# Performance work log

Hardware: AMD Instinct MI355X
Metric: run time of the kernel (lower is better)

## Reference

```python
import jax, jax.numpy as jnp
import numpy as np

L, N, D, B_, T = 4, 4, 2048, 2, 2048  # num_blocks, expansion_rate, dim, batch, seq


def setup_inputs() -> dict:
    key = jax.random.key(0)
    ks = jax.random.split(key, 12)
    f = lambda k, sh, s=0.02: s * jax.random.normal(k, sh, jnp.float32)
    x = jax.random.normal(ks[0], (B_, T, D), jnp.float32)
    # structural torch inits + small noise so grads/kernels are exercised
    eyecols = jnp.stack([jnp.eye(N, dtype=jnp.float32)[:, [i % N]] for i in range(L)])  # [L,N,1]
    A_m = eyecols + f(ks[1], (L, N, 1), 0.05)
    A_r = jnp.broadcast_to(jnp.eye(N, dtype=jnp.float32), (L, N, N)) + f(ks[2], (L, N, N), 0.05)
    Bp = jnp.ones((L, 1, N), jnp.float32) + f(ks[3], (L, 1, N), 0.05)
    W_m = f(ks[4], (L, D, 1))
    W_r = f(ks[5], (L, D, N))
    W_b = f(ks[6], (L, D, N))
    s_a = 0.01 * jnp.ones((L, 1, 1), jnp.float32)
    s_b = 0.01 * jnp.ones((L, 1, 1), jnp.float32)
    dyn_gamma = jnp.ones((L, D), jnp.float32) + f(ks[7], (L, D), 0.05)   # LayerNorm(bias=False)
    norm_gamma = jnp.ones((L, D), jnp.float32) + f(ks[8], (L, D), 0.05)  # per-block norm weight
    norm_beta = f(ks[9], (L, D))                                          # per-block norm bias
    Wblk = f(ks[10], (L, D, D), 1.0) / np.sqrt(D)                         # block = Linear(D, D)
    bblk = f(ks[11], (L, D))
    return dict(x=x, A_m=A_m, A_r=A_r, Bp=Bp, W_m=W_m, W_r=W_r, W_b=W_b,
                s_a=s_a, s_b=s_b, dyn_gamma=dyn_gamma, norm_gamma=norm_gamma,
                norm_beta=norm_beta, Wblk=Wblk, bblk=bblk)


def _ln(x, gamma, beta=None, eps=1e-5):
    mu = jnp.mean(x, axis=-1, keepdims=True)
    var = jnp.mean(jnp.square(x - mu), axis=-1, keepdims=True)
    y = (x - mu) * jax.lax.rsqrt(var + eps) * gamma
    return y if beta is None else y + beta


def reference(x, A_m, A_r, Bp, W_m, W_r, W_b, s_a, s_b,
              dyn_gamma, norm_gamma, norm_beta, Wblk, bblk):
    # hyper branch (n > 0), dynamic=True, pre_norm=True
    H = jnp.repeat(x[:, :, None, :], N, axis=2)  # [B,T,N,D]
    for i in range(L):
        # ---- width connections ----
        Hn = _ln(H, dyn_gamma[i])                                              # dynamic LN, no bias
        Am = A_m[i] + s_a[i] * jnp.tanh(jnp.einsum('btnd,do->btno', Hn, W_m[i]))  # [B,T,N,1]
        Ar = A_r[i] + s_a[i] * jnp.tanh(jnp.einsum('btnd,dm->btnm', Hn, W_r[i]))  # [B,T,N,N]
        WC = jnp.concatenate([Am, Ar], axis=-1)                                # [B,T,N,1+N]
        Ht = jnp.einsum('btnd,btnm->btdm', H, WC)                              # H^T @ WC
        h = Ht[..., 0]                                                         # [B,T,D]
        H = jnp.swapaxes(Ht[..., 1:], -2, -1)                                  # [B,T,N,D]
        # ---- pre-norm + block ----
        h = _ln(h, norm_gamma[i], norm_beta[i])
        h = jnp.einsum('btd,de->bte', h, Wblk[i]) + bblk[i]
        # ---- depth connections ----
        hn = _ln(h, dyn_gamma[i])
        Bv = Bp[i][0] + s_b[i] * jnp.tanh(jnp.einsum('btd,dn->btn', hn, W_b[i]))  # [B,T,N]
        H = H + h[:, :, None, :] * Bv[..., None]
    return H.sum(axis=2)  # [B,T,D]
```

## Files before the change

kernel.cpp:

```cpp
#include <hip/hip_runtime.h>
#include <hip/hip_bf16.h>


#define DD 2048
#define NN 4
#define LL 4
#define NTOK 4096
#define EPSF 1e-5f

typedef __attribute__((ext_vector_type(8))) short bf16x8;
typedef __attribute__((ext_vector_type(4))) float f32x4;
typedef __attribute__((ext_vector_type(2))) float f32x2;

__device__ __forceinline__ float bf2f(short u) {
  union { unsigned int i; float f; } v;
  v.i = ((unsigned int)(unsigned short)u) << 16;
  return v.f;
}
__device__ __forceinline__ short f2bf(float f) {
  __hip_bfloat16 h = __float2bfloat16(f);
  short s;
  __builtin_memcpy(&s, &h, 2);
  return s;
}
__device__ __forceinline__ float wred(float v) {
#pragma unroll
  for (int off = 32; off > 0; off >>= 1) v += __shfl_xor(v, off, 64);
  return v;
}
__device__ __forceinline__ void ld16(const void* g, void* l) {
  __builtin_amdgcn_global_load_lds(
      (const __attribute__((address_space(1))) void*)g,
      (__attribute__((address_space(3))) void*)l, 16, 0, 0);
}

__global__ __launch_bounds__(256) void prep_pack(
    const float* __restrict__ W_m, const float* __restrict__ W_r,
    const float* __restrict__ W_b, const float* __restrict__ dyn_gamma,
    const float* __restrict__ norm_gamma, const float* __restrict__ norm_beta,
    short* __restrict__ gwm, short* __restrict__ gwr, short* __restrict__ gwb,
    float* __restrict__ rb) {
  const int i = blockIdx.x * 256 + threadIdx.x;
  const float g = dyn_gamma[i];
  gwm[i] = f2bf(g * W_m[i]);
  f32x4 r = *(const f32x4*)(W_r + (size_t)i * 4);
  f32x4 b = *(const f32x4*)(W_b + (size_t)i * 4);
  short ro[4], bo[4];
#pragma unroll
  for (int k = 0; k < 4; k++) { ro[k] = f2bf(g * r[k]); bo[k] = f2bf(g * b[k]); }
  *(unsigned long long*)(gwr + (size_t)i * 4) = *(unsigned long long*)ro;
  *(unsigned long long*)(gwb + (size_t)i * 4) = *(unsigned long long*)bo;
  rb[i] = norm_beta[i] / norm_gamma[i];
}

__global__ __launch_bounds__(64) void prep_sums(
    const float* __restrict__ W_m, const float* __restrict__ W_r,
    const float* __restrict__ W_b, const float* __restrict__ dyn_gamma,
    float* __restrict__ S0w, float* __restrict__ T0d) {
  const int l = blockIdx.x;
  const int lane = threadIdx.x;
  float s[5] = {0, 0, 0, 0, 0}, t[4] = {0, 0, 0, 0};
  for (int d = lane; d < DD; d += 64) {
    const float g = dyn_gamma[l * DD + d];
    s[0] += g * W_m[l * DD + d];
    f32x4 r = *(const f32x4*)(W_r + ((size_t)l * DD + d) * 4);
    f32x4 b = *(const f32x4*)(W_b + ((size_t)l * DD + d) * 4);
#pragma unroll
    for (int m = 0; m < 4; m++) { s[1 + m] += g * r[m]; t[m] += g * b[m]; }
  }
#pragma unroll
  for (int m = 0; m < 5; m++) s[m] = wred(s[m]);
#pragma unroll
  for (int n = 0; n < 4; n++) t[n] = wred(t[n]);
  if (lane == 0) {
#pragma unroll
    for (int m = 0; m < 5; m++) S0w[l * 5 + m] = s[m];
#pragma unroll
    for (int n = 0; n < 4; n++) T0d[l * 4 + n] = t[n];
  }
}

__global__ __launch_bounds__(256) void transpose_wblk(
    const float* __restrict__ W, const float* __restrict__ norm_gamma,
    short* __restrict__ Wt) {
  __shared__ float tile[64][65];
  const int blk = blockIdx.z;
  const int c0 = blockIdx.x * 64;
  const int r0 = blockIdx.y * 64;
  const float* Ws = W + (size_t)blk * DD * DD;
  short* Wd = Wt + (size_t)blk * DD * DD;
  const int tx = threadIdx.x & 63, ty = threadIdx.x >> 6;
#pragma unroll
  for (int r = 0; r < 16; r++) {
    const int row = ty + r * 4;
    tile[row][tx] = Ws[(size_t)(r0 + row) * DD + c0 + tx];
  }
  const float gsc = norm_gamma[blk * DD + r0 + tx];
  __syncthreads();
#pragma unroll
  for (int r = 0; r < 16; r++) {
    const int row = ty + r * 4;
    Wd[(size_t)(c0 + row) * DD + r0 + tx] = f2bf(tile[tx][row] * gsc);
  }
}

__global__ __launch_bounds__(256) void row_sums(
    const short* __restrict__ Wt, const float* __restrict__ rb,
    const float* __restrict__ bblk, float* __restrict__ E0,
    float* __restrict__ E1) {
  const int l = blockIdx.y;
  const int e = blockIdx.x * 4 + (threadIdx.x >> 6);
  const int lane = threadIdx.x & 63;
  const short* row = Wt + ((size_t)l * DD + e) * DD;
  const float* rbl = rb + l * DD;
  float s1 = 0.f, s0 = 0.f;
#pragma unroll
  for (int it = 0; it < 4; it++) {
    const int d0 = lane * 8 + it * 512;
    bf16x8 w = *(const bf16x8*)(row + d0);
    f32x4 r0 = *(const f32x4*)(rbl + d0), r1 = *(const f32x4*)(rbl + d0 + 4);
#pragma unroll
    for (int q = 0; q < 8; q++) {
      const float wq = bf2f(w[q]);
      s1 += wq;
      s0 += wq * ((q < 4) ? r0[q] : r1[q - 4]);
    }
  }
  s1 = wred(s1); s0 = wred(s0);
  if (lane == 0) {
    E1[l * DD + e] = s1;
    E0[l * DD + e] = s0 + bblk[l * DD + e];
  }
}

__global__ __launch_bounds__(256) void width0_kernel(
    const float* __restrict__ x, short* __restrict__ Hst,
    short* __restrict__ hout, f32x2* __restrict__ tst,
    const float* __restrict__ A_m, const float* __restrict__ A_r,
    const short* __restrict__ gwm, const short* __restrict__ gwr,
    const float* __restrict__ s_a, const float* __restrict__ S0w) {
  const int wave = threadIdx.x >> 6;
  const int lane = threadIdx.x & 63;
  const int tok = blockIdx.x * 4 + wave;
  const int blk = 0;
  const short* wm = gwm + blk * DD;
  const short* wr = gwr + (size_t)blk * DD * 4;

  bf16x8 hreg[4];
  const float* xr = x + (size_t)tok * DD;
#pragma unroll
  for (int j = 0; j < 4; j++) {
    const int d0 = lane * 8 + j * 512;
    f32x4 a = *(const f32x4*)(xr + d0);
    f32x4 b = *(const f32x4*)(xr + d0 + 4);
    bf16x8 p;
#pragma unroll
    for (int q = 0; q < 4; q++) { p[q] = f2bf(a[q]); p[4 + q] = f2bf(b[q]); }
    hreg[j] = p;
  }

  float sH = 0, sH2 = 0, S1[5] = {0, 0, 0, 0, 0};
#pragma unroll
  for (int j = 0; j < 4; j++) {
    const int d0 = lane * 8 + j * 512;
    bf16x8 mv = *(const bf16x8*)(wm + d0);
    bf16x8 wv[4];
#pragma unroll
    for (int p = 0; p < 4; p++)
      wv[p] = *(const bf16x8*)(wr + (size_t)(d0 + 2 * p) * 4);
#pragma unroll
    for (int q = 0; q < 8; q++) {
      const float hv = bf2f(hreg[j][q]);
      sH += hv; sH2 += hv * hv;
      S1[0] += hv * bf2f(mv[q]);
#pragma unroll
      for (int m = 0; m < 4; m++)
        S1[1 + m] += hv * bf2f(wv[q >> 1][(q & 1) * 4 + m]);
    }
  }
  sH = wred(sH); sH2 = wred(sH2);
#pragma unroll
  for (int m = 0; m < 5; m++) S1[m] = wred(S1[m]);

  const float sa = s_a[blk];
  const float mu0 = sH * (1.f / DD);
  const float inv0 = rsqrtf(sH2 * (1.f / DD) - mu0 * mu0 + EPSF);
  float amSum = 0.f, arCol[NN] = {0, 0, 0, 0};
  {
    const float t0 = tanhf(inv0 * (S1[0] - mu0 * S0w[blk * 5 + 0]));
    float tm[NN];
#pragma unroll
    for (int m = 0; m < NN; m++)
      tm[m] = tanhf(inv0 * (S1[1 + m] - mu0 * S0w[blk * 5 + 1 + m]));
#pragma unroll
    for (int n = 0; n < NN; n++) {
      amSum += A_m[blk * NN + n] + sa * t0;
#pragma unroll
      for (int m = 0; m < NN; m++)
        arCol[m] += A_r[blk * NN * NN + n * NN + m] + sa * tm[m];
    }
  }

  short* Ho = Hst + (size_t)tok * NN * DD;
  short* hw = hout + (size_t)tok * DD;
  float sh = 0.f, sh2 = 0.f;
#pragma unroll
  for (int j = 0; j < 4; j++) {
    const int d0 = lane * 8 + j * 512;
    bf16x8 outp[NN], ho;
#pragma unroll
    for (int q = 0; q < 8; q++) {
      const float hv = bf2f(hreg[j][q]);
      const float a0 = hv * amSum;
      sh += a0; sh2 += a0 * a0;
      ho[q] = f2bf(a0);
#pragma unroll
      for (int m = 0; m < NN; m++) outp[m][q] = f2bf(hv * arCol[m]);
    }
    *(bf16x8*)(hw + d0) = ho;
#pragma unroll
    for (int m = 0; m < NN; m++) *(bf16x8*)(Ho + m * DD + d0) = outp[m];
  }
  sh = wred(sh); sh2 = wred(sh2);
  if (lane == 0) {
    const float mu = sh * (1.f / DD);
    const float inv = rsqrtf(sh2 * (1.f / DD) - mu * mu + EPSF);
    f32x2 t; t[0] = inv; t[1] = mu * inv;
    tst[tok] = t;
  }
}

__global__ __launch_bounds__(256) void gemm_kernel(
    const short* __restrict__ A, const short* __restrict__ Bt,
    const f32x2* __restrict__ tst, const float* __restrict__ E0,
    const float* __restrict__ E1, short* __restrict__ C) {
  __shared__ short lA[2][128 * 64];
  __shared__ short lB[2][128 * 64];
  const int tid = threadIdx.x;
  const int lane = tid & 63;
  const int wave = tid >> 6;
  const int m0 = blockIdx.x * 128, n0 = blockIdx.y * 128;
  const int wm = wave >> 1, wn = wave & 1;

  f32x4 acc[4][4] = {};

#define STAGE(buf, kt)                                                        \
  {                                                                           \
    const int k0 = (kt) * 64;                                                 \
    _Pragma("unroll") for (int c = 0; c < 4; c++) {                           \
      const int idx = c * 256 + tid;                                          \
      const int row = idx >> 3;                                               \
      const int colsw = (((idx & 7) ^ (row & 7)) * 8);                        \
      ld16(A + (size_t)(m0 + row) * DD + k0 + colsw,                          \
           (char*)&lA[buf][0] + idx * 16);                                    \
      ld16(Bt + (size_t)(n0 + row) * DD + k0 + colsw,                         \
           (char*)&lB[buf][0] + idx * 16);                                    \
    }                                                                         \
  }

  STAGE(0, 0);
  __syncthreads();

  for (int kt = 0; kt < 32; ++kt) {
    const int cur = kt & 1;
    if (kt < 31) STAGE(cur ^ 1, kt + 1);
    const char* bufA = (const char*)&lA[cur][0];
    const char* bufB = (const char*)&lB[cur][0];
#pragma unroll
    for (int kk = 0; kk < 2; ++kk) {
      const int gsw = (kk * 64 + (lane >> 4) * 16) ^ ((lane & 7) << 4);
      bf16x8 af[4], bfr[4];
#pragma unroll
      for (int m = 0; m < 4; m++) {
        const int r = wm * 64 + m * 16 + (lane & 15);
        af[m] = *(const bf16x8*)(bufA + r * 128 + gsw);
      }
#pragma unroll
      for (int n = 0; n < 4; n++) {
        const int r = wn * 64 + n * 16 + (lane & 15);
        bfr[n] = *(const bf16x8*)(bufB + r * 128 + gsw);
      }
#pragma unroll
      for (int m = 0; m < 4; m++)
#pragma unroll
        for (int n = 0; n < 4; n++)
          acc[m][n] = __builtin_amdgcn_mfma_f32_16x16x32_bf16(
              af[m], bfr[n], acc[m][n], 0, 0, 0);
    }
    __syncthreads();
  }
#undef STAGE

  float e0c[4], e1c[4];
  int cols[4];
#pragma unroll
  for (int n = 0; n < 4; n++) {
    cols[n] = n0 + wn * 64 + n * 16 + (lane & 15);
    e0c[n] = E0[cols[n]];
    e1c[n] = E1[cols[n]];
  }
#pragma unroll
  for (int m = 0; m < 4; m++) {
    const int rbase = m0 + wm * 64 + m * 16 + ((lane >> 4) << 2);
#pragma unroll
    for (int j = 0; j < 4; j++) {
      const int row = rbase + j;
      const f32x2 iv = tst[row];
#pragma unroll
      for (int n = 0; n < 4; n++)
        C[(size_t)row * DD + cols[n]] =
            f2bf(iv[0] * acc[m][n][j] - iv[1] * e1c[n] + e0c[n]);
    }
  }
}

__global__ __launch_bounds__(256) void fused_dw(
    const short* __restrict__ h2, short* __restrict__ Hst,
    short* __restrict__ hout, f32x2* __restrict__ tst,
    const float* __restrict__ Bp, const short* __restrict__ gwb,
    const float* __restrict__ s_b, const float* __restrict__ A_m,
    const float* __restrict__ A_r, const short* __restrict__ gwm,
    const short* __restrict__ gwr, const float* __restrict__ s_a,
    const float* __restrict__ S0w, const float* __restrict__ T0d, int blk) {
  const int wave = threadIdx.x >> 6;
  const int lane = threadIdx.x & 63;
  const int tok = blockIdx.x * 4 + wave;
  const int nblk = blk + 1;
  const short* hr = h2 + (size_t)tok * DD;
  short* Ho = Hst + (size_t)tok * NN * DD;

  bf16x8 h2r[4], hold[NN][4];
#pragma unroll
  for (int j = 0; j < 4; j++) {
    const int d0 = lane * 8 + j * 512;
    h2r[j] = *(const bf16x8*)(hr + d0);
#pragma unroll
    for (int n = 0; n < NN; n++)
      hold[n][j] = *(const bf16x8*)(Ho + n * DD + d0);
  }

  const short* wb = gwb + (size_t)blk * DD * 4;
  float s1 = 0.f, s2 = 0.f, T1[NN] = {0, 0, 0, 0};
#pragma unroll
  for (int j = 0; j < 4; j++) {
    const int d0 = lane * 8 + j * 512;
    bf16x8 wv[4];
#pragma unroll
    for (int p = 0; p < 4; p++)
      wv[p] = *(const bf16x8*)(wb + (size_t)(d0 + 2 * p) * 4);
#pragma unroll
    for (int q = 0; q < 8; q++) {
      const float hv = bf2f(h2r[j][q]);
      s1 += hv; s2 += hv * hv;
#pragma unroll
      for (int n = 0; n < NN; n++)
        T1[n] += hv * bf2f(wv[q >> 1][(q & 1) * 4 + n]);
    }
  }
  s1 = wred(s1); s2 = wred(s2);
#pragma unroll
  for (int n = 0; n < NN; n++) T1[n] = wred(T1[n]);
  float Bv[NN];
  {
    const float mu = s1 * (1.f / DD);
    const float inv = rsqrtf(s2 * (1.f / DD) - mu * mu + EPSF);
    const float sb = s_b[blk];
#pragma unroll
    for (int n = 0; n < NN; n++)
      Bv[n] = Bp[blk * NN + n] +
              sb * tanhf(inv * (T1[n] - mu * T0d[blk * NN + n]));
  }
#pragma unroll
  for (int n = 0; n < NN; n++)
#pragma unroll
    for (int j = 0; j < 4; j++) {
      bf16x8 o;
#pragma unroll
      for (int q = 0; q < 8; q++)
        o[q] = f2bf(bf2f(hold[n][j][q]) + bf2f(h2r[j][q]) * Bv[n]);
      hold[n][j] = o;
    }

  const short* wm = gwm + nblk * DD;
  const short* wr = gwr + (size_t)nblk * DD * 4;
  float sH[NN] = {0, 0, 0, 0}, sH2[NN] = {0, 0, 0, 0};
  float S1[NN][5];
#pragma unroll
  for (int n = 0; n < NN; n++)
#pragma unroll
    for (int m = 0; m < 5; m++) S1[n][m] = 0.f;

#pragma unroll
  for (int j = 0; j < 4; j++) {
    const int d0 = lane * 8 + j * 512;
    bf16x8 mv = *(const bf16x8*)(wm + d0);
    bf16x8 wv[4];
#pragma unroll
    for (int p = 0; p < 4; p++)
      wv[p] = *(const bf16x8*)(wr + (size_t)(d0 + 2 * p) * 4);
#pragma unroll
    for (int q = 0; q < 8; q++) {
      float gw[5];
      gw[0] = bf2f(mv[q]);
#pragma unroll
      for (int m = 0; m < 4; m++)
        gw[1 + m] = bf2f(wv[q >> 1][(q & 1) * 4 + m]);
#pragma unroll
      for (int n = 0; n < NN; n++) {
        const float hv = bf2f(hold[n][j][q]);
        sH[n] += hv; sH2[n] += hv * hv;
#pragma unroll
        for (int m = 0; m < 5; m++) S1[n][m] += hv * gw[m];
      }
    }
  }
#pragma unroll
  for (int n = 0; n < NN; n++) { sH[n] = wred(sH[n]); sH2[n] = wred(sH2[n]); }
#pragma unroll
  for (int n = 0; n < NN; n++)
#pragma unroll
    for (int m = 0; m < 5; m++) S1[n][m] = wred(S1[n][m]);

  const float sa = s_a[nblk];
  float Am[NN], Ar[NN][NN];
#pragma unroll
  for (int n = 0; n < NN; n++) {
    const float mu = sH[n] * (1.f / DD);
    const float var = sH2[n] * (1.f / DD) - mu * mu;
    const float inv = rsqrtf(var + EPSF);
    Am[n] = A_m[nblk * NN + n] +
            sa * tanhf(inv * (S1[n][0] - mu * S0w[nblk * 5 + 0]));
#pragma unroll
    for (int m = 0; m < NN; m++)
      Ar[n][m] = A_r[nblk * NN * NN + n * NN + m] +
                 sa * tanhf(inv * (S1[n][1 + m] - mu * S0w[nblk * 5 + 1 + m]));
  }

  short* hw = hout + (size_t)tok * DD;
  float sh = 0.f, sh2 = 0.f;
#pragma unroll
  for (int j = 0; j < 4; j++) {
    const int d0 = lane * 8 + j * 512;
    bf16x8 outp[NN], ho;
#pragma unroll
    for (int q = 0; q < 8; q++) {
      float a0 = 0.f, am0 = 0.f, am1 = 0.f, am2 = 0.f, am3 = 0.f;
#pragma unroll
      for (int n = 0; n < NN; n++) {
        const float hv = bf2f(hold[n][j][q]);
        a0 += hv * Am[n];
        am0 += hv * Ar[n][0];
        am1 += hv * Ar[n][1];
        am2 += hv * Ar[n][2];
        am3 += hv * Ar[n][3];
      }
      sh += a0; sh2 += a0 * a0;
      ho[q] = f2bf(a0);
      outp[0][q] = f2bf(am0); outp[1][q] = f2bf(am1);
      outp[2][q] = f2bf(am2); outp[3][q] = f2bf(am3);
    }
    *(bf16x8*)(hw + d0) = ho;
#pragma unroll
    for (int m = 0; m < NN; m++) *(bf16x8*)(Ho + m * DD + d0) = outp[m];
  }
  sh = wred(sh); sh2 = wred(sh2);
  if (lane == 0) {
    const float mu = sh * (1.f / DD);
    const float inv = rsqrtf(sh2 * (1.f / DD) - mu * mu + EPSF);
    f32x2 t; t[0] = inv; t[1] = mu * inv;
    tst[tok] = t;
  }
}

__global__ __launch_bounds__(256) void depth_last(
    const short* __restrict__ h2, const short* __restrict__ Hst,
    float* __restrict__ out, const float* __restrict__ Bp,
    const short* __restrict__ gwb, const float* __restrict__ s_b,
    const float* __restrict__ T0d, int blk) {
  const int wave = threadIdx.x >> 6;
  const int lane = threadIdx.x & 63;
  const int tok = blockIdx.x * 4 + wave;
  const short* hr = h2 + (size_t)tok * DD;
  const short* wb = gwb + (size_t)blk * DD * 4;

  bf16x8 h2r[4];
  float s1 = 0.f, s2 = 0.f, T1[NN] = {0, 0, 0, 0};
#pragma unroll
  for (int j = 0; j < 4; j++) {
    const int d0 = lane * 8 + j * 512;
    h2r[j] = *(const bf16x8*)(hr + d0);
    bf16x8 wv[4];
#pragma unroll
    for (int p = 0; p < 4; p++)
      wv[p] = *(const bf16x8*)(wb + (size_t)(d0 + 2 * p) * 4);
#pragma unroll
    for (int q = 0; q < 8; q++) {
      const float hv = bf2f(h2r[j][q]);
      s1 += hv; s2 += hv * hv;
#pragma unroll
      for (int n = 0; n < NN; n++)
        T1[n] += hv * bf2f(wv[q >> 1][(q & 1) * 4 + n]);
    }
  }
  s1 = wred(s1); s2 = wred(s2);
#pragma unroll
  for (int n = 0; n < NN; n++) T1[n] = wred(T1[n]);
  const float mu = s1 * (1.f / DD);
  const float inv = rsqrtf(s2 * (1.f / DD) - mu * mu + EPSF);
  const float sb = s_b[blk];
  float bsum = 0.f;
#pragma unroll
  for (int n = 0; n < NN; n++)
    bsum += Bp[blk * NN + n] + sb * tanhf(inv * (T1[n] - mu * T0d[blk * NN + n]));

  const short* Ho = Hst + (size_t)tok * NN * DD;
  float* orow = out + (size_t)tok * DD;
#pragma unroll
  for (int j = 0; j < 4; j++) {
    const int d0 = lane * 8 + j * 512;
    bf16x8 hrow[NN];
#pragma unroll
    for (int n = 0; n < NN; n++) hrow[n] = *(const bf16x8*)(Ho + n * DD + d0);
    f32x4 o0, o1;
#pragma unroll
    for (int q = 0; q < 8; q++) {
      const float hv = bf2f(h2r[j][q]);
      float s = hv * bsum;
#pragma unroll
      for (int n = 0; n < NN; n++) s += bf2f(hrow[n][q]);
      if (q < 4) o0[q] = s; else o1[q - 4] = s;
    }
    *(f32x4*)(orow + d0) = o0;
    *(f32x4*)(orow + d0 + 4) = o1;
  }
}

extern "C" void kernel_launch(void* const* d_in, const int* in_sizes, int n_in,
                              void* d_out, int out_size, void* d_ws,
                              size_t ws_size, hipStream_t stream) {
  const float* x = (const float*)d_in[0];
  const float* A_m = (const float*)d_in[1];
  const float* A_r = (const float*)d_in[2];
  const float* Bp = (const float*)d_in[3];
  const float* W_m = (const float*)d_in[4];
  const float* W_r = (const float*)d_in[5];
  const float* W_b = (const float*)d_in[6];
  const float* s_a = (const float*)d_in[7];
  const float* s_b = (const float*)d_in[8];
  const float* dyn_gamma = (const float*)d_in[9];
  const float* norm_gamma = (const float*)d_in[10];
  const float* norm_beta = (const float*)d_in[11];
  const float* Wblk = (const float*)d_in[12];
  const float* bblk = (const float*)d_in[13];
  float* out = (float*)d_out;

  char* ws = (char*)d_ws;
  short* Hst = (short*)(ws);
  short* hbuf = (short*)(ws + 67108864);
  short* h2 = (short*)(ws + 83886080);
  char* aux = ws + 100663296;
  short* gwm = (short*)(aux);
  short* gwr = (short*)(aux + 16384);
  short* gwb = (short*)(aux + 16384 + 65536);
  float* rb = (float*)(aux + 16384 + 131072);
  float* S0w = (float*)(aux + 16384 + 131072 + 32768);
  float* T0d = (float*)(aux + 16384 + 131072 + 32768 + 128);
  f32x2* tst = (f32x2*)(aux + 16384 + 131072 + 32768 + 256);
  float* E0 = (float*)(aux + 16384 + 131072 + 32768 + 256 + 32768);
  float* E1 = E0 + LL * DD;
  short* Wt = (short*)d_out;

  dim3 tb(256);
  prep_pack<<<32, tb, 0, stream>>>(W_m, W_r, W_b, dyn_gamma, norm_gamma,
                                   norm_beta, gwm, gwr, gwb, rb);
  prep_sums<<<4, dim3(64), 0, stream>>>(W_m, W_r, W_b, dyn_gamma, S0w, T0d);
  transpose_wblk<<<dim3(32, 32, 4), tb, 0, stream>>>(Wblk, norm_gamma, Wt);
  row_sums<<<dim3(512, 4), tb, 0, stream>>>(Wt, rb, bblk, E0, E1);
  width0_kernel<<<1024, tb, 0, stream>>>(x, Hst, hbuf, tst, A_m, A_r, gwm,
                                         gwr, s_a, S0w);
  for (int i = 0; i < LL; i++) {
    gemm_kernel<<<dim3(32, 16), tb, 0, stream>>>(
        hbuf, Wt + (size_t)i * DD * DD, tst, E0 + i * DD, E1 + i * DD, h2);
    if (i < LL - 1)
      fused_dw<<<1024, tb, 0, stream>>>(h2, Hst, hbuf, tst, Bp, gwb, s_b, A_m,
                                        A_r, gwm, gwr, s_a, S0w, T0d, i);
    else
      depth_last<<<1024, tb, 0, stream>>>(h2, Hst, out, Bp, gwb, s_b, T0d, i);
  }
}
```

Before: 390.8 us.

## Fold depth update algebraically into width statistics and widen GEMM to 8 waves

The fused depth/width kernel no longer materialises the depth-updated H before computing the width LayerNorm statistics and projections. It gathers sums over the old H and h2 in one pass and reconstructs the updated mean, variance and projections algebraically from cross terms weighted by Bv. The depth contribution is folded into the width mixing coefficients, so the bf16 rounding of H+h*Bv is skipped and results can differ slightly. Separately, the GEMM kernel moves to 512 threads (8 waves, each with a 64x32 tile), which halves per-thread accumulators and may change occupancy and LDS read traffic.

```diff
diff --git a/kernel.cpp b/kernel.cpp
--- a/kernel.cpp
+++ b/kernel.cpp
@@ -230,7 +230,7 @@
   }
 }
 
-__global__ __launch_bounds__(256) void gemm_kernel(
+__global__ __launch_bounds__(512) void gemm_kernel(
     const short* __restrict__ A, const short* __restrict__ Bt,
     const f32x2* __restrict__ tst, const float* __restrict__ E0,
     const float* __restrict__ E1, short* __restrict__ C) {
@@ -240,15 +240,16 @@
   const int lane = tid & 63;
   const int wave = tid >> 6;
   const int m0 = blockIdx.x * 128, n0 = blockIdx.y * 128;
-  const int wm = wave >> 1, wn = wave & 1;
-
-  f32x4 acc[4][4] = {};
+  const int wm = wave >> 2;
+  const int wn = wave & 3;
+
+  f32x4 acc[4][2] = {};
 
 #define STAGE(buf, kt)                                                        \
   {                                                                           \
     const int k0 = (kt) * 64;                                                 \
-    _Pragma("unroll") for (int c = 0; c < 4; c++) {                           \
-      const int idx = c * 256 + tid;                                          \
+    _Pragma("unroll") for (int c = 0; c < 2; c++) {                           \
+      const int idx = c * 512 + tid;                                          \
       const int row = idx >> 3;                                               \
       const int colsw = (((idx & 7) ^ (row & 7)) * 8);                        \
       ld16(A + (size_t)(m0 + row) * DD + k0 + colsw,                          \
@@ -269,21 +270,21 @@
 #pragma unroll
     for (int kk = 0; kk < 2; ++kk) {
       const int gsw = (kk * 64 + (lane >> 4) * 16) ^ ((lane & 7) << 4);
-      bf16x8 af[4], bfr[4];
+      bf16x8 af[4], bfr[2];
 #pragma unroll
       for (int m = 0; m < 4; m++) {
         const int r = wm * 64 + m * 16 + (lane & 15);
         af[m] = *(const bf16x8*)(bufA + r * 128 + gsw);
       }
 #pragma unroll
-      for (int n = 0; n < 4; n++) {
-        const int r = wn * 64 + n * 16 + (lane & 15);
+      for (int n = 0; n < 2; n++) {
+        const int r = wn * 32 + n * 16 + (lane & 15);
         bfr[n] = *(const bf16x8*)(bufB + r * 128 + gsw);
       }
 #pragma unroll
       for (int m = 0; m < 4; m++)
 #pragma unroll
-        for (int n = 0; n < 4; n++)
+        for (int n = 0; n < 2; n++)
           acc[m][n] = __builtin_amdgcn_mfma_f32_16x16x32_bf16(
               af[m], bfr[n], acc[m][n], 0, 0, 0);
     }
@@ -291,11 +292,11 @@
   }
 #undef STAGE
 
-  float e0c[4], e1c[4];
-  int cols[4];
-#pragma unroll
-  for (int n = 0; n < 4; n++) {
-    cols[n] = n0 + wn * 64 + n * 16 + (lane & 15);
+  float e0c[2], e1c[2];
+  int cols[2];
+#pragma unroll
+  for (int n = 0; n < 2; n++) {
+    cols[n] = n0 + wn * 32 + n * 16 + (lane & 15);
     e0c[n] = E0[cols[n]];
     e1c[n] = E1[cols[n]];
   }
@@ -307,7 +308,7 @@
       const int row = rbase + j;
       const f32x2 iv = tst[row];
 #pragma unroll
-      for (int n = 0; n < 4; n++)
+      for (int n = 0; n < 2; n++)
         C[(size_t)row * DD + cols[n]] =
             f2bf(iv[0] * acc[m][n][j] - iv[1] * e1c[n] + e0c[n]);
     }
@@ -340,100 +341,100 @@
   }
 
   const short* wb = gwb + (size_t)blk * DD * 4;
-  float s1 = 0.f, s2 = 0.f, T1[NN] = {0, 0, 0, 0};
-#pragma unroll
-  for (int j = 0; j < 4; j++) {
-    const int d0 = lane * 8 + j * 512;
-    bf16x8 wv[4];
-#pragma unroll
-    for (int p = 0; p < 4; p++)
-      wv[p] = *(const bf16x8*)(wb + (size_t)(d0 + 2 * p) * 4);
-#pragma unroll
-    for (int q = 0; q < 8; q++) {
-      const float hv = bf2f(h2r[j][q]);
-      s1 += hv; s2 += hv * hv;
+  const short* wm = gwm + nblk * DD;
+  const short* wr = gwr + (size_t)nblk * DD * 4;
+
+  float s1 = 0.f, s2 = 0.f;
+  float T1[NN] = {0, 0, 0, 0}, U1[5] = {0, 0, 0, 0, 0}, Cx[NN] = {0, 0, 0, 0};
+  float sH[NN] = {0, 0, 0, 0}, sH2[NN] = {0, 0, 0, 0};
+  float S1[NN][5];
+#pragma unroll
+  for (int n = 0; n < NN; n++)
+#pragma unroll
+    for (int m = 0; m < 5; m++) S1[n][m] = 0.f;
+
+#pragma unroll
+  for (int j = 0; j < 4; j++) {
+    const int d0 = lane * 8 + j * 512;
+    bf16x8 mv = *(const bf16x8*)(wm + d0);
+    bf16x8 wv[4], bv[4];
+#pragma unroll
+    for (int p = 0; p < 4; p++) {
+      wv[p] = *(const bf16x8*)(wr + (size_t)(d0 + 2 * p) * 4);
+      bv[p] = *(const bf16x8*)(wb + (size_t)(d0 + 2 * p) * 4);
+    }
+#pragma unroll
+    for (int q = 0; q < 8; q++) {
+      const float hv2 = bf2f(h2r[j][q]);
+      s1 += hv2; s2 += hv2 * hv2;
+      float gw[5];
+      gw[0] = bf2f(mv[q]);
+#pragma unroll
+      for (int m = 0; m < 4; m++)
+        gw[1 + m] = bf2f(wv[q >> 1][(q & 1) * 4 + m]);
 #pragma unroll
       for (int n = 0; n < NN; n++)
-        T1[n] += hv * bf2f(wv[q >> 1][(q & 1) * 4 + n]);
+        T1[n] += hv2 * bf2f(bv[q >> 1][(q & 1) * 4 + n]);
+#pragma unroll
+      for (int m = 0; m < 5; m++) U1[m] += hv2 * gw[m];
+#pragma unroll
+      for (int n = 0; n < NN; n++) {
+        const float hvn = bf2f(hold[n][j][q]);
+        Cx[n] += hvn * hv2;
+        sH[n] += hvn; sH2[n] += hvn * hvn;
+#pragma unroll
+        for (int m = 0; m < 5; m++) S1[n][m] += hvn * gw[m];
+      }
     }
   }
   s1 = wred(s1); s2 = wred(s2);
 #pragma unroll
-  for (int n = 0; n < NN; n++) T1[n] = wred(T1[n]);
+  for (int n = 0; n < NN; n++) {
+    T1[n] = wred(T1[n]); Cx[n] = wred(Cx[n]);
+    sH[n] = wred(sH[n]); sH2[n] = wred(sH2[n]);
+  }
+#pragma unroll
+  for (int m = 0; m < 5; m++) U1[m] = wred(U1[m]);
+#pragma unroll
+  for (int n = 0; n < NN; n++)
+#pragma unroll
+    for (int m = 0; m < 5; m++) S1[n][m] = wred(S1[n][m]);
+
   float Bv[NN];
   {
-    const float mu = s1 * (1.f / DD);
-    const float inv = rsqrtf(s2 * (1.f / DD) - mu * mu + EPSF);
+    const float mu2 = s1 * (1.f / DD);
+    const float inv2 = rsqrtf(s2 * (1.f / DD) - mu2 * mu2 + EPSF);
     const float sb = s_b[blk];
 #pragma unroll
     for (int n = 0; n < NN; n++)
       Bv[n] = Bp[blk * NN + n] +
-              sb * tanhf(inv * (T1[n] - mu * T0d[blk * NN + n]));
-  }
-#pragma unroll
-  for (int n = 0; n < NN; n++)
-#pragma unroll
-    for (int j = 0; j < 4; j++) {
-      bf16x8 o;
-#pragma unroll
-      for (int q = 0; q < 8; q++)
-        o[q] = f2bf(bf2f(hold[n][j][q]) + bf2f(h2r[j][q]) * Bv[n]);
-      hold[n][j] = o;
-    }
-
-  const short* wm = gwm + nblk * DD;
-  const short* wr = gwr + (size_t)nblk * DD * 4;
-  float sH[NN] = {0, 0, 0, 0}, sH2[NN] = {0, 0, 0, 0};
-  float S1[NN][5];
-#pragma unroll
-  for (int n = 0; n < NN; n++)
-#pragma unroll
-    for (int m = 0; m < 5; m++) S1[n][m] = 0.f;
-
-#pragma unroll
-  for (int j = 0; j < 4; j++) {
-    const int d0 = lane * 8 + j * 512;
-    bf16x8 mv = *(const bf16x8*)(wm + d0);
-    bf16x8 wv[4];
-#pragma unroll
-    for (int p = 0; p < 4; p++)
-      wv[p] = *(const bf16x8*)(wr + (size_t)(d0 + 2 * p) * 4);
-#pragma unroll
-    for (int q = 0; q < 8; q++) {
-      float gw[5];
-      gw[0] = bf2f(mv[q]);
-#pragma unroll
-      for (int m = 0; m < 4; m++)
-        gw[1 + m] = bf2f(wv[q >> 1][(q & 1) * 4 + m]);
-#pragma unroll
-      for (int n = 0; n < NN; n++) {
-        const float hv = bf2f(hold[n][j][q]);
-        sH[n] += hv; sH2[n] += hv * hv;
-#pragma unroll
-        for (int m = 0; m < 5; m++) S1[n][m] += hv * gw[m];
-      }
-    }
-  }
-#pragma unroll
-  for (int n = 0; n < NN; n++) { sH[n] = wred(sH[n]); sH2[n] = wred(sH2[n]); }
-#pragma unroll
-  for (int n = 0; n < NN; n++)
-#pragma unroll
-    for (int m = 0; m < 5; m++) S1[n][m] = wred(S1[n][m]);
+              sb * tanhf(inv2 * (T1[n] - mu2 * T0d[blk * NN + n]));
+  }
 
   const float sa = s_a[nblk];
   float Am[NN], Ar[NN][NN];
 #pragma unroll
   for (int n = 0; n < NN; n++) {
-    const float mu = sH[n] * (1.f / DD);
-    const float var = sH2[n] * (1.f / DD) - mu * mu;
-    const float inv = rsqrtf(var + EPSF);
+    const float sHp = sH[n] + Bv[n] * s1;
+    const float sH2p = sH2[n] + 2.f * Bv[n] * Cx[n] + Bv[n] * Bv[n] * s2;
+    const float mu = sHp * (1.f / DD);
+    const float inv = rsqrtf(sH2p * (1.f / DD) - mu * mu + EPSF);
+    const float S10 = S1[n][0] + Bv[n] * U1[0];
     Am[n] = A_m[nblk * NN + n] +
-            sa * tanhf(inv * (S1[n][0] - mu * S0w[nblk * 5 + 0]));
-#pragma unroll
-    for (int m = 0; m < NN; m++)
+            sa * tanhf(inv * (S10 - mu * S0w[nblk * 5 + 0]));
+#pragma unroll
+    for (int m = 0; m < NN; m++) {
+      const float S1m = S1[n][1 + m] + Bv[n] * U1[1 + m];
       Ar[n][m] = A_r[nblk * NN * NN + n * NN + m] +
-                 sa * tanhf(inv * (S1[n][1 + m] - mu * S0w[nblk * 5 + 1 + m]));
+                 sa * tanhf(inv * (S1m - mu * S0w[nblk * 5 + 1 + m]));
+    }
+  }
+  float ca = 0.f, cr[NN] = {0, 0, 0, 0};
+#pragma unroll
+  for (int n = 0; n < NN; n++) {
+    ca += Bv[n] * Am[n];
+#pragma unroll
+    for (int m = 0; m < NN; m++) cr[m] += Bv[n] * Ar[n][m];
   }
 
   short* hw = hout + (size_t)tok * DD;
@@ -444,15 +445,18 @@
     bf16x8 outp[NN], ho;
 #pragma unroll
     for (int q = 0; q < 8; q++) {
-      float a0 = 0.f, am0 = 0.f, am1 = 0.f, am2 = 0.f, am3 = 0.f;
+      const float hv2 = bf2f(h2r[j][q]);
+      float a0 = hv2 * ca;
+      float am0 = hv2 * cr[0], am1 = hv2 * cr[1];
+      float am2 = hv2 * cr[2], am3 = hv2 * cr[3];
 #pragma unroll
       for (int n = 0; n < NN; n++) {
-        const float hv = bf2f(hold[n][j][q]);
-        a0 += hv * Am[n];
-        am0 += hv * Ar[n][0];
-        am1 += hv * Ar[n][1];
-        am2 += hv * Ar[n][2];
-        am3 += hv * Ar[n][3];
+        const float hvn = bf2f(hold[n][j][q]);
+        a0 += hvn * Am[n];
+        am0 += hvn * Ar[n][0];
+        am1 += hvn * Ar[n][1];
+        am2 += hvn * Ar[n][2];
+        am3 += hvn * Ar[n][3];
       }
       sh += a0; sh2 += a0 * a0;
       ho[q] = f2bf(a0);
@@ -579,7 +583,7 @@
   width0_kernel<<<1024, tb, 0, stream>>>(x, Hst, hbuf, tst, A_m, A_r, gwm,
                                          gwr, s_a, S0w);
   for (int i = 0; i < LL; i++) {
-    gemm_kernel<<<dim3(32, 16), tb, 0, stream>>>(
+    gemm_kernel<<<dim3(32, 16), dim3(512), 0, stream>>>(
         hbuf, Wt + (size_t)i * DD * DD, tst, E0 + i * DD, E1 + i * DD, h2);
     if (i < LL - 1)
       fused_dw<<<1024, tb, 0, stream>>>(h2, Hst, hbuf, tst, Bp, gwb, s_b, A_m,
```

Measured after the change: 479.5 us. +22.7%, slower.
